# Performance work log

Hardware: AMD Instinct MI355X
Metric: run time of the kernel (lower is better)

The kernel has to match this reference:

```python
import jax, jax.numpy as jnp
import numpy as np

N_NODES = 50000
N_EDGES = 800000
NUM_HEADS = 4
HEAD_DIM = 32
IN_DIM = 128
NEG_SLOPE = 0.2


def setup_inputs() -> dict:
    key = jax.random.key(0)
    k1, k2, k3, k4, k5, k6 = jax.random.split(key, 6)
    x = jax.random.normal(k1, (N_NODES, IN_DIM), dtype=jnp.float32)
    W = jax.random.normal(k2, (NUM_HEADS * HEAD_DIM, IN_DIM), dtype=jnp.float32) * 0.05
    attn_l = jax.random.normal(k3, (NUM_HEADS, HEAD_DIM), dtype=jnp.float32) * 0.05
    attn_r = jax.random.normal(k4, (NUM_HEADS, HEAD_DIM), dtype=jnp.float32) * 0.05
    src = jax.random.randint(k5, (N_EDGES,), 0, N_NODES, dtype=jnp.int32)
    dst = jnp.sort(jax.random.randint(k6, (N_EDGES,), 0, N_NODES, dtype=jnp.int32))
    return {"x": x, "W": W, "attn_l": attn_l, "attn_r": attn_r, "src": src, "dst": dst}


def reference(x, W, attn_l, attn_r, src, dst):
    N = x.shape[0]
    H, D = attn_l.shape
    # linear projection: [N, H*D] -> [N, H, D]
    feat = (x @ W.T).reshape(N, H, D)
    # per-node attention terms  [N, H]
    el = jnp.einsum('nhd,hd->nh', feat, attn_l)
    er = jnp.einsum('nhd,hd->nh', feat, attn_r)
    # per-edge logits (u_add_v) + leaky relu  [E, H]
    e = el[src] + er[dst]
    e = jnp.where(e > 0, e, NEG_SLOPE * e)
    # edge softmax segmented by destination node
    e_max = jax.ops.segment_max(e, dst, num_segments=N)          # [N, H]
    e_exp = jnp.exp(e - e_max[dst])                              # [E, H]
    denom = jax.ops.segment_sum(e_exp, dst, num_segments=N)     # [N, H]
    alpha = e_exp / denom[dst]                                   # [E, H]
    # attention-weighted neighbor aggregation  [N, H, D]
    out = jax.ops.segment_sum(alpha[:, :, None] * feat[src], dst, num_segments=N)
    return out.reshape(N, H * D)
```

## Files before the change

kernel.cpp:

```cpp
#include <hip/hip_runtime.h>
#include <math.h>

#define NN 50000
#define NE 800000
#define NH 4
#define HD 32
#define FD 128
#define NTILE 3125

typedef __attribute__((ext_vector_type(8))) short short8;
typedef __attribute__((ext_vector_type(4))) float floatx4;

__device__ __forceinline__ unsigned short f2bf(float f) {
    union { float f; unsigned u; } v; v.f = f;
    unsigned u = v.u;
    return (unsigned short)((u + 0x7FFFu + ((u >> 16) & 1u)) >> 16);
}
__device__ __forceinline__ float bf_lo(unsigned u) {
    union { unsigned u; float f; } v; v.u = u << 16; return v.f;
}
__device__ __forceinline__ float bf_hi(unsigned u) {
    union { unsigned u; float f; } v; v.u = u & 0xFFFF0000u; return v.f;
}

__global__ __launch_bounds__(512) void k_gemm_fused(const float* __restrict__ x,
                                                    const float* __restrict__ W,
                                                    const float* __restrict__ al,
                                                    const float* __restrict__ ar,
                                                    unsigned short* __restrict__ feat_bf,
                                                    float* __restrict__ el,
                                                    float* __restrict__ er) {
    __shared__ unsigned short Wl[FD * 136];
    const int tid = threadIdx.x;

    for (int p = tid; p < FD * 64; p += 512) {
        int c = p >> 6, k2 = (p & 63) * 2;
        float2 wv = *(const float2*)&W[c * FD + k2];
        *(unsigned*)&Wl[c * 136 + k2] =
            (unsigned)f2bf(wv.x) | ((unsigned)f2bf(wv.y) << 16);
    }
    __syncthreads();

    const int wv_id = tid >> 6, lane = tid & 63;
    const int col = lane & 15, quad = lane >> 4;

    float alr[8], arr[8];
    #pragma unroll
    for (int ct = 0; ct < 8; ++ct) {
        alr[ct] = al[col + 16 * ct];
        arr[ct] = ar[col + 16 * ct];
    }

    for (int tile = blockIdx.x * 8 + wv_id; tile < NTILE; tile += gridDim.x * 8) {
        const int n0 = tile * 16;

        short8 afrag[4];
        const float* xrow = x + (size_t)(n0 + col) * FD;
        #pragma unroll
        for (int s = 0; s < 4; ++s) {
            float4 u0 = *(const float4*)&xrow[s * 32 + quad * 8];
            float4 u1 = *(const float4*)&xrow[s * 32 + quad * 8 + 4];
            short8 a;
            a[0] = (short)f2bf(u0.x); a[1] = (short)f2bf(u0.y);
            a[2] = (short)f2bf(u0.z); a[3] = (short)f2bf(u0.w);
            a[4] = (short)f2bf(u1.x); a[5] = (short)f2bf(u1.y);
            a[6] = (short)f2bf(u1.z); a[7] = (short)f2bf(u1.w);
            afrag[s] = a;
        }

        floatx4 acc[8];
        #pragma unroll
        for (int ct = 0; ct < 8; ++ct) acc[ct] = (floatx4){0.f, 0.f, 0.f, 0.f};

        #pragma unroll
        for (int ct = 0; ct < 8; ++ct) {
            #pragma unroll
            for (int s = 0; s < 4; ++s) {
                short8 b = *(const short8*)&Wl[(ct * 16 + col) * 136 + s * 32 + quad * 8];
                acc[ct] = __builtin_amdgcn_mfma_f32_16x16x32_bf16(afrag[s], b, acc[ct], 0, 0, 0);
            }
        }

        #pragma unroll
        for (int ct = 0; ct < 8; ++ct) {
            #pragma unroll
            for (int r = 0; r < 4; ++r) {
                feat_bf[(size_t)(n0 + quad * 4 + r) * FD + ct * 16 + col] = f2bf(acc[ct][r]);
            }
        }

        #pragma unroll
        for (int r = 0; r < 4; ++r) {
            float ev[8];
            #pragma unroll
            for (int hh = 0; hh < NH; ++hh) {
                ev[hh]     = acc[2 * hh][r] * alr[2 * hh] + acc[2 * hh + 1][r] * alr[2 * hh + 1];
                ev[4 + hh] = acc[2 * hh][r] * arr[2 * hh] + acc[2 * hh + 1][r] * arr[2 * hh + 1];
            }
            #pragma unroll
            for (int m = 1; m < 16; m <<= 1) {
                #pragma unroll
                for (int j = 0; j < 8; ++j) ev[j] += __shfl_xor(ev[j], m);
            }
            if (col == 0) {
                int n = n0 + quad * 4 + r;
                *(float4*)&el[n * NH] = make_float4(ev[0], ev[1], ev[2], ev[3]);
                *(float4*)&er[n * NH] = make_float4(ev[4], ev[5], ev[6], ev[7]);
            }
        }
    }
}

__global__ void k_edgew(const float* __restrict__ el,
                        const float* __restrict__ er,
                        const int* __restrict__ src,
                        const int* __restrict__ dst,
                        float* __restrict__ wE,
                        int* __restrict__ rows) {
    int e = blockIdx.x * blockDim.x + threadIdx.x;
    if (e >= NE) return;
    int sj = src[e], dj = dst[e];

    if (e == 0) {
        for (int n = 0; n <= dj; ++n) rows[n] = 0;
    } else {
        int prev = dst[e - 1];
        for (int n = prev + 1; n <= dj; ++n) rows[n] = e;
    }
    if (e == NE - 1) {
        for (int n = dj + 1; n <= NN; ++n) rows[n] = NE;
    }

    float4 el4 = *(const float4*)&el[sj * NH];
    float4 er4 = *(const float4*)&er[dj * NH];
    float4 w;
    float lg, z;
    lg = el4.x + er4.x; z = fmaxf(lg, 0.2f * lg); w.x = __expf(z);
    lg = el4.y + er4.y; z = fmaxf(lg, 0.2f * lg); w.y = __expf(z);
    lg = el4.z + er4.z; z = fmaxf(lg, 0.2f * lg); w.z = __expf(z);
    lg = el4.w + er4.w; z = fmaxf(lg, 0.2f * lg); w.w = __expf(z);
    *(float4*)&wE[e * NH] = w;
}

__global__ __launch_bounds__(256) void k_aggregate(const unsigned short* __restrict__ feat_bf,
                                                   const float* __restrict__ wE,
                                                   const int* __restrict__ src,
                                                   const int* __restrict__ rows,
                                                   float* __restrict__ out) {
    const int wave = threadIdx.x >> 6;
    const int lane = threadIdx.x & 63;
    const int n = blockIdx.x * 4 + wave;
    if (n >= NN) return;

    const int s = rows[n], t = rows[n + 1];
    const int q  = lane >> 4;
    const int lp = lane & 15;
    const int h  = lp >> 2;
    const int dimoff = 8 * lp;

    float acc[8] = {0.f, 0.f, 0.f, 0.f, 0.f, 0.f, 0.f, 0.f};
    float den = 0.f;

    for (int e = s; e < t; e += 16) {
        int   sjv[4];
        float wv4[4];
        #pragma unroll
        for (int u = 0; u < 4; ++u) {
            int ei = e + 4 * u + q;
            int ec = (ei < t) ? ei : (t - 1);
            sjv[u] = src[ec];
            wv4[u] = (ei < t) ? wE[ec * NH + h] : 0.f;
        }
        uint4 uvv[4];
        #pragma unroll
        for (int u = 0; u < 4; ++u)
            uvv[u] = *(const uint4*)&feat_bf[(size_t)sjv[u] * FD + dimoff];
        #pragma unroll
        for (int u = 0; u < 4; ++u) {
            float w = wv4[u];
            uint4 uv = uvv[u];
            acc[0] += w * bf_lo(uv.x); acc[1] += w * bf_hi(uv.x);
            acc[2] += w * bf_lo(uv.y); acc[3] += w * bf_hi(uv.y);
            acc[4] += w * bf_lo(uv.z); acc[5] += w * bf_hi(uv.z);
            acc[6] += w * bf_lo(uv.w); acc[7] += w * bf_hi(uv.w);
            den += w;
        }
    }

    #pragma unroll
    for (int m = 16; m < 64; m <<= 1) {
        #pragma unroll
        for (int j = 0; j < 8; ++j) acc[j] += __shfl_xor(acc[j], m);
        den += __shfl_xor(den, m);
    }

    if (q == 0) {
        const float rden = (den > 0.f) ? 1.f / den : 0.f;
        float* op = out + (size_t)n * FD + dimoff;
        *(float4*)op       = make_float4(acc[0] * rden, acc[1] * rden, acc[2] * rden, acc[3] * rden);
        *(float4*)(op + 4) = make_float4(acc[4] * rden, acc[5] * rden, acc[6] * rden, acc[7] * rden);
    }
}

extern "C" void kernel_launch(void* const* d_in, const int* in_sizes, int n_in,
                              void* d_out, int out_size, void* d_ws, size_t ws_size,
                              hipStream_t stream) {
    const float* x  = (const float*)d_in[0];
    const float* W  = (const float*)d_in[1];
    const float* al = (const float*)d_in[2];
    const float* ar = (const float*)d_in[3];
    const int* src  = (const int*)d_in[4];
    const int* dst  = (const int*)d_in[5];
    float* out = (float*)d_out;

    unsigned short* feat_bf = (unsigned short*)d_ws;
    float* el = (float*)(feat_bf + (size_t)NN * FD);
    float* er = el + (size_t)NN * NH;
    int*   rows = (int*)(er + (size_t)NN * NH);
    float* wE = (float*)(((uintptr_t)(rows + NN + 1) + 15) & ~(uintptr_t)15);

    k_gemm_fused<<<256, 512, 0, stream>>>(x, W, al, ar, feat_bf, el, er);
    k_edgew<<<(NE + 255) / 256, 256, 0, stream>>>(el, er, src, dst, wE, rows);
    k_aggregate<<<(NN + 3) / 4, 256, 0, stream>>>(feat_bf, wE, src, rows, out);
}
```

Before: 133.8 us.

## Fuse row-offset build into GEMM launch and compute edge weights inside aggregation

The separate edge-weight kernel is removed. The CSR row-offset construction now runs as extra blocks of the GEMM launch, and the exp(leaky_relu(el+er)) weight is recomputed per edge inside the aggregation kernel. This drops one kernel launch and the write and re-read of the per-edge weight buffer. In exchange, aggregation does an extra gather of el per edge plus the exp. The src loads are vectorized with aligned int4 reads, and the GEMM grid is one tile per wave instead of a grid-stride loop.

Result: slower. 142.2 us (+6.3%).

```diff
diff --git a/kernel.cpp b/kernel.cpp
--- a/kernel.cpp
+++ b/kernel.cpp
@@ -7,6 +7,8 @@
 #define HD 32
 #define FD 128
 #define NTILE 3125
+#define GEMM_BLOCKS 391
+#define ROWS_BLOCKS ((NE + 511) / 512)
 
 typedef __attribute__((ext_vector_type(8))) short short8;
 typedef __attribute__((ext_vector_type(4))) float floatx4;
@@ -23,16 +25,35 @@
     union { unsigned u; float f; } v; v.u = u & 0xFFFF0000u; return v.f;
 }
 
-__global__ __launch_bounds__(512) void k_gemm_fused(const float* __restrict__ x,
-                                                    const float* __restrict__ W,
-                                                    const float* __restrict__ al,
-                                                    const float* __restrict__ ar,
-                                                    unsigned short* __restrict__ feat_bf,
-                                                    float* __restrict__ el,
-                                                    float* __restrict__ er) {
+__global__ __launch_bounds__(512) void k_gemm_rows(const float* __restrict__ x,
+                                                   const float* __restrict__ W,
+                                                   const float* __restrict__ al,
+                                                   const float* __restrict__ ar,
+                                                   const int* __restrict__ dst,
+                                                   unsigned short* __restrict__ feat_bf,
+                                                   float* __restrict__ el,
+                                                   float* __restrict__ er,
+                                                   int* __restrict__ rows) {
+    const int tid = threadIdx.x;
+
+    if (blockIdx.x >= GEMM_BLOCKS) {
+        int e = (blockIdx.x - GEMM_BLOCKS) * 512 + tid;
+        if (e < NE) {
+            int dj = dst[e];
+            if (e == 0) {
+                for (int n = 0; n <= dj; ++n) rows[n] = 0;
+            } else {
+                int prev = dst[e - 1];
+                for (int n = prev + 1; n <= dj; ++n) rows[n] = e;
+            }
+            if (e == NE - 1) {
+                for (int n = dj + 1; n <= NN; ++n) rows[n] = NE;
+            }
+        }
+        return;
+    }
+
     __shared__ unsigned short Wl[FD * 136];
-    const int tid = threadIdx.x;
-
     for (int p = tid; p < FD * 64; p += 512) {
         int c = p >> 6, k2 = (p & 63) * 2;
         float2 wv = *(const float2*)&W[c * FD + k2];
@@ -42,6 +63,8 @@
     __syncthreads();
 
     const int wv_id = tid >> 6, lane = tid & 63;
+    const int tile = blockIdx.x * 8 + wv_id;
+    if (tile >= NTILE) return;
     const int col = lane & 15, quad = lane >> 4;
 
     float alr[8], arr[8];
@@ -51,99 +74,67 @@
         arr[ct] = ar[col + 16 * ct];
     }
 
-    for (int tile = blockIdx.x * 8 + wv_id; tile < NTILE; tile += gridDim.x * 8) {
-        const int n0 = tile * 16;
-
-        short8 afrag[4];
-        const float* xrow = x + (size_t)(n0 + col) * FD;
+    const int n0 = tile * 16;
+
+    short8 afrag[4];
+    const float* xrow = x + (size_t)(n0 + col) * FD;
+    #pragma unroll
+    for (int s = 0; s < 4; ++s) {
+        float4 u0 = *(const float4*)&xrow[s * 32 + quad * 8];
+        float4 u1 = *(const float4*)&xrow[s * 32 + quad * 8 + 4];
+        short8 a;
+        a[0] = (short)f2bf(u0.x); a[1] = (short)f2bf(u0.y);
+        a[2] = (short)f2bf(u0.z); a[3] = (short)f2bf(u0.w);
+        a[4] = (short)f2bf(u1.x); a[5] = (short)f2bf(u1.y);
+        a[6] = (short)f2bf(u1.z); a[7] = (short)f2bf(u1.w);
+        afrag[s] = a;
+    }
+
+    floatx4 acc[8];
+    #pragma unroll
+    for (int ct = 0; ct < 8; ++ct) acc[ct] = (floatx4){0.f, 0.f, 0.f, 0.f};
+
+    #pragma unroll
+    for (int ct = 0; ct < 8; ++ct) {
         #pragma unroll
         for (int s = 0; s < 4; ++s) {
-            float4 u0 = *(const float4*)&xrow[s * 32 + quad * 8];
-            float4 u1 = *(const float4*)&xrow[s * 32 + quad * 8 + 4];
-            short8 a;
-            a[0] = (short)f2bf(u0.x); a[1] = (short)f2bf(u0.y);
-            a[2] = (short)f2bf(u0.z); a[3] = (short)f2bf(u0.w);
-            a[4] = (short)f2bf(u1.x); a[5] = (short)f2bf(u1.y);
-            a[6] = (short)f2bf(u1.z); a[7] = (short)f2bf(u1.w);
-            afrag[s] = a;
-        }
-
-        floatx4 acc[8];
-        #pragma unroll
-        for (int ct = 0; ct < 8; ++ct) acc[ct] = (floatx4){0.f, 0.f, 0.f, 0.f};
-
-        #pragma unroll
-        for (int ct = 0; ct < 8; ++ct) {
+            short8 b = *(const short8*)&Wl[(ct * 16 + col) * 136 + s * 32 + quad * 8];
+            acc[ct] = __builtin_amdgcn_mfma_f32_16x16x32_bf16(afrag[s], b, acc[ct], 0, 0, 0);
+        }
+    }
+
+    #pragma unroll
+    for (int ct = 0; ct < 8; ++ct) {
+        #pragma unroll
+        for (int r = 0; r < 4; ++r) {
+            feat_bf[(size_t)(n0 + quad * 4 + r) * FD + ct * 16 + col] = f2bf(acc[ct][r]);
+        }
+    }
+
+    #pragma unroll
+    for (int r = 0; r < 4; ++r) {
+        float ev[8];
+        #pragma unroll
+        for (int hh = 0; hh < NH; ++hh) {
+            ev[hh]     = acc[2 * hh][r] * alr[2 * hh] + acc[2 * hh + 1][r] * alr[2 * hh + 1];
+            ev[4 + hh] = acc[2 * hh][r] * arr[2 * hh] + acc[2 * hh + 1][r] * arr[2 * hh + 1];
+        }
+        #pragma unroll
+        for (int m = 1; m < 16; m <<= 1) {
             #pragma unroll
-            for (int s = 0; s < 4; ++s) {
-                short8 b = *(const short8*)&Wl[(ct * 16 + col) * 136 + s * 32 + quad * 8];
-                acc[ct] = __builtin_amdgcn_mfma_f32_16x16x32_bf16(afrag[s], b, acc[ct], 0, 0, 0);
-            }
-        }
-
-        #pragma unroll
-        for (int ct = 0; ct < 8; ++ct) {
-            #pragma unroll
-            for (int r = 0; r < 4; ++r) {
-                feat_bf[(size_t)(n0 + quad * 4 + r) * FD + ct * 16 + col] = f2bf(acc[ct][r]);
-            }
-        }
-
-        #pragma unroll
-        for (int r = 0; r < 4; ++r) {
-            float ev[8];
-            #pragma unroll
-            for (int hh = 0; hh < NH; ++hh) {
-                ev[hh]     = acc[2 * hh][r] * alr[2 * hh] + acc[2 * hh + 1][r] * alr[2 * hh + 1];
-                ev[4 + hh] = acc[2 * hh][r] * arr[2 * hh] + acc[2 * hh + 1][r] * arr[2 * hh + 1];
-            }
-            #pragma unroll
-            for (int m = 1; m < 16; m <<= 1) {
-                #pragma unroll
-                for (int j = 0; j < 8; ++j) ev[j] += __shfl_xor(ev[j], m);
-            }
-            if (col == 0) {
-                int n = n0 + quad * 4 + r;
-                *(float4*)&el[n * NH] = make_float4(ev[0], ev[1], ev[2], ev[3]);
-                *(float4*)&er[n * NH] = make_float4(ev[4], ev[5], ev[6], ev[7]);
-            }
-        }
-    }
-}
-
-__global__ void k_edgew(const float* __restrict__ el,
-                        const float* __restrict__ er,
-                        const int* __restrict__ src,
-                        const int* __restrict__ dst,
-                        float* __restrict__ wE,
-                        int* __restrict__ rows) {
-    int e = blockIdx.x * blockDim.x + threadIdx.x;
-    if (e >= NE) return;
-    int sj = src[e], dj = dst[e];
-
-    if (e == 0) {
-        for (int n = 0; n <= dj; ++n) rows[n] = 0;
-    } else {
-        int prev = dst[e - 1];
-        for (int n = prev + 1; n <= dj; ++n) rows[n] = e;
-    }
-    if (e == NE - 1) {
-        for (int n = dj + 1; n <= NN; ++n) rows[n] = NE;
-    }
-
-    float4 el4 = *(const float4*)&el[sj * NH];
-    float4 er4 = *(const float4*)&er[dj * NH];
-    float4 w;
-    float lg, z;
-    lg = el4.x + er4.x; z = fmaxf(lg, 0.2f * lg); w.x = __expf(z);
-    lg = el4.y + er4.y; z = fmaxf(lg, 0.2f * lg); w.y = __expf(z);
-    lg = el4.z + er4.z; z = fmaxf(lg, 0.2f * lg); w.z = __expf(z);
-    lg = el4.w + er4.w; z = fmaxf(lg, 0.2f * lg); w.w = __expf(z);
-    *(float4*)&wE[e * NH] = w;
+            for (int j = 0; j < 8; ++j) ev[j] += __shfl_xor(ev[j], m);
+        }
+        if (col == 0) {
+            int n = n0 + quad * 4 + r;
+            *(float4*)&el[n * NH] = make_float4(ev[0], ev[1], ev[2], ev[3]);
+            *(float4*)&er[n * NH] = make_float4(ev[4], ev[5], ev[6], ev[7]);
+        }
+    }
 }
 
 __global__ __launch_bounds__(256) void k_aggregate(const unsigned short* __restrict__ feat_bf,
-                                                   const float* __restrict__ wE,
+                                                   const float* __restrict__ el,
+                                                   const float* __restrict__ er,
                                                    const int* __restrict__ src,
                                                    const int* __restrict__ rows,
                                                    float* __restrict__ out) {
@@ -152,38 +143,60 @@
     const int n = blockIdx.x * 4 + wave;
     if (n >= NN) return;
 
-    const int s = rows[n], t = rows[n + 1];
+    const int s = __builtin_amdgcn_readfirstlane(rows[n]);
+    const int t = __builtin_amdgcn_readfirstlane(rows[n + 1]);
     const int q  = lane >> 4;
     const int lp = lane & 15;
     const int h  = lp >> 2;
     const int dimoff = 8 * lp;
 
+    const float erh = er[n * NH + h];
+
     float acc[8] = {0.f, 0.f, 0.f, 0.f, 0.f, 0.f, 0.f, 0.f};
     float den = 0.f;
 
-    for (int e = s; e < t; e += 16) {
-        int   sjv[4];
-        float wv4[4];
+    for (int e = (s & ~3); e < t; e += 16) {
+        const int base = e + 4 * q;
+        int sj4[4];
+        const bool full4 = (base >= s) && (base + 3 < t);
+        if (full4) {
+            int4 sv = *(const int4*)&src[base];
+            sj4[0] = sv.x; sj4[1] = sv.y; sj4[2] = sv.z; sj4[3] = sv.w;
+        } else {
+            #pragma unroll
+            for (int u = 0; u < 4; ++u) {
+                int ei = base + u;
+                sj4[u] = (ei >= s && ei < t) ? src[ei] : 0;
+            }
+        }
+
+        float elv[4];
         #pragma unroll
         for (int u = 0; u < 4; ++u) {
-            int ei = e + 4 * u + q;
-            int ec = (ei < t) ? ei : (t - 1);
-            sjv[u] = src[ec];
-            wv4[u] = (ei < t) ? wE[ec * NH + h] : 0.f;
+            int ei = base + u;
+            if (ei >= s && ei < t) elv[u] = el[sj4[u] * NH + h];
         }
         uint4 uvv[4];
         #pragma unroll
-        for (int u = 0; u < 4; ++u)
-            uvv[u] = *(const uint4*)&feat_bf[(size_t)sjv[u] * FD + dimoff];
-        #pragma unroll
         for (int u = 0; u < 4; ++u) {
-            float w = wv4[u];
-            uint4 uv = uvv[u];
-            acc[0] += w * bf_lo(uv.x); acc[1] += w * bf_hi(uv.x);
-            acc[2] += w * bf_lo(uv.y); acc[3] += w * bf_hi(uv.y);
-            acc[4] += w * bf_lo(uv.z); acc[5] += w * bf_hi(uv.z);
-            acc[6] += w * bf_lo(uv.w); acc[7] += w * bf_hi(uv.w);
-            den += w;
+            int ei = base + u;
+            if (ei >= s && ei < t)
+                uvv[u] = *(const uint4*)&feat_bf[(size_t)sj4[u] * FD + dimoff];
+        }
+
+        #pragma unroll
+        for (int u = 0; u < 4; ++u) {
+            int ei = base + u;
+            if (ei >= s && ei < t) {
+                float lg = elv[u] + erh;
+                float w = __expf(fmaxf(lg, 0.2f * lg));
+                uint4 uv = uvv[u];
+                acc[0] += w * bf_lo(uv.x); acc[1] += w * bf_hi(uv.x);
+                acc[2] += w * bf_lo(uv.y); acc[3] += w * bf_hi(uv.y);
+                acc[4] += w * bf_lo(uv.z); acc[5] += w * bf_hi(uv.z);
+                acc[6] += w * bf_lo(uv.w); acc[7] += w * bf_hi(uv.w);
+                den += w;
+            }
         }
     }
 
@@ -217,9 +230,8 @@
     float* el = (float*)(feat_bf + (size_t)NN * FD);
     float* er = el + (size_t)NN * NH;
     int*   rows = (int*)(er + (size_t)NN * NH);
-    float* wE = (float*)(((uintptr_t)(rows + NN + 1) + 15) & ~(uintptr_t)15);
-
-    k_gemm_fused<<<256, 512, 0, stream>>>(x, W, al, ar, feat_bf, el, er);
-    k_edgew<<<(NE + 255) / 256, 256, 0, stream>>>(el, er, src, dst, wE, rows);
-    k_aggregate<<<(NN + 3) / 4, 256, 0, stream>>>(feat_bf, wE, src, rows, out);
-}
+
+    k_gemm_rows<<<GEMM_BLOCKS + ROWS_BLOCKS, 512, 0, stream>>>(x, W, al, ar, dst,
+                                                               feat_bf, el, er, rows);
+    k_aggregate<<<(NN + 3) / 4, 256, 0, stream>>>(feat_bf, el, er, src, rows, out);
+}
```
